# Performance work log

Hardware: AMD Instinct MI355X
Metric: run time of the kernel (lower is better)

The kernel has to match this reference:

```python
import jax, jax.numpy as jnp
import numpy as np

B, S, IN, H, D, STATE, PRED = 256, 512, 32, 256, 32, 4, 96


def setup_inputs() -> dict:
    key = jax.random.key(0)
    ks = jax.random.split(key, 16)
    sc = 1.0 / np.sqrt(H)

    def u(k, shape):
        return jax.random.uniform(k, shape, jnp.float32, -sc, sc)

    return {
        "x": jax.random.normal(ks[0], (B, S, IN), jnp.float32),
        # GRU layer 0
        "W_ih_l0": u(ks[1], (3 * H, IN)),
        "W_hh_l0": u(ks[2], (3 * H, H)),
        "b_ih_l0": u(ks[3], (3 * H,)),
        "b_hh_l0": u(ks[4], (3 * H,)),
        # GRU layer 1
        "W_ih_l1": u(ks[5], (3 * H, H)),
        "W_hh_l1": u(ks[6], (3 * H, H)),
        "b_ih_l1": u(ks[7], (3 * H,)),
        "b_hh_l1": u(ks[8], (3 * H,)),
        # state projection: hidden -> STATE*output_dim
        "W_proj": u(ks[9], (STATE * D, H)),
        "b_proj": u(ks[10], (STATE * D,)),
        # observation matrix, eye-initialized (output_dim, STATE)
        "C": jnp.eye(D, STATE, dtype=jnp.float32),
        "raw_level_decay": jnp.zeros((D,), jnp.float32),
        "raw_trend_decay": jnp.zeros((D,), jnp.float32),
        "raw_gamma": jnp.zeros((D,), jnp.float32),
        "omega": jnp.zeros((D,), jnp.float32),
    }


def _gru_layer(xs, W_ih, W_hh, b_ih, b_hh):
    # xs: (B, S, in_dim). Precompute input projections as one big GEMM.
    xp = jnp.einsum('bsi,gi->bsg', xs, W_ih) + b_ih  # (B, S, 3H)

    def step(h, xt):
        gh = h @ W_hh.T + b_hh  # (B, 3H)
        xr, xz, xn = jnp.split(xt, 3, axis=-1)
        hr, hz, hn = jnp.split(gh, 3, axis=-1)
        r = jax.nn.sigmoid(xr + hr)
        z = jax.nn.sigmoid(xz + hz)
        n = jnp.tanh(xn + r * hn)
        h_new = (1.0 - z) * n + z * h
        return h_new, h_new

    h0 = jnp.zeros((xs.shape[0], W_hh.shape[1]), xs.dtype)
    _, hs = jax.lax.scan(step, h0, jnp.swapaxes(xp, 0, 1))  # (S, B, H)
    return jnp.swapaxes(hs, 0, 1)  # (B, S, H)


def reference(x, W_ih_l0, W_hh_l0, b_ih_l0, b_hh_l0,
              W_ih_l1, W_hh_l1, b_ih_l1, b_hh_l1,
              W_proj, b_proj, C,
              raw_level_decay, raw_trend_decay, raw_gamma, omega):
    h1 = _gru_layer(x, W_ih_l0, W_hh_l0, b_ih_l0, b_hh_l0)
    h2 = _gru_layer(h1, W_ih_l1, W_hh_l1, b_ih_l1, b_hh_l1)
    final_h = h2[:, -1, :]  # (B, H)

    d_out = C.shape[0]
    s = (final_h @ W_proj.T + b_proj).reshape(x.shape[0], d_out, STATE)  # (B, D, 4)

    # time-invariant block-diagonal transition coefficients
    a_l = jax.nn.sigmoid(raw_level_decay) * 0.15 + 0.85
    a_t = jax.nn.sigmoid(raw_trend_decay) * 0.25 + 0.7
    g = jax.nn.sigmoid(raw_gamma) * 0.2 + 0.8
    c, sn = jnp.cos(omega), jnp.sin(omega)
    rot00, rot01 = g * c, -g * sn
    rot10, rot11 = g * sn, g * c

    def step(s, _):
        new_s = jnp.stack([
            s[..., 0] * a_l,
            s[..., 1] * a_t,
            s[..., 2] * rot00 + s[..., 3] * rot10,
            s[..., 2] * rot01 + s[..., 3] * rot11,
        ], axis=-1)
        y = jnp.einsum('ds,bds->bd', C, new_s)
        return new_s, y

    _, ys = jax.lax.scan(step, s, None, length=PRED)  # (PRED, B, D)
    return jnp.swapaxes(ys, 0, 1)  # (B, PRED, D)
```

## Files before the change

kernel.cpp:

```cpp
#include <hip/hip_runtime.h>
#include <cstdio>
#include <cstdint>

typedef _Float16 f16;
typedef f16 hf2   __attribute__((ext_vector_type(2)));
typedef f16 f16x8 __attribute__((ext_vector_type(8)));
typedef float f32x4 __attribute__((ext_vector_type(4)));
typedef unsigned int   u32;
typedef unsigned short u16;

#define B_    256
#define S_    512
#define IN_   32
#define H_    256
#define G3_   768
#define D_    32
#define PRED_ 96
#define TC_   32
#define KP_   72

#if __has_builtin(__builtin_amdgcn_fdot2)
__device__ __forceinline__ float fdot2(hf2 a, hf2 b, float c) {
  return __builtin_amdgcn_fdot2(a, b, c, false);
}
#else
__device__ __forceinline__ float fdot2(hf2 a, hf2 b, float c) {
  return c + (float)a[0] * (float)b[0] + (float)a[1] * (float)b[1];
}
#endif

__device__ __forceinline__ float sigm(float x) {
  return __builtin_amdgcn_rcpf(1.f + __expf(-x));
}
__device__ __forceinline__ float tanh_fast(float x) {
  return 1.f - 2.f * __builtin_amdgcn_rcpf(__expf(2.f * x) + 1.f);
}
__device__ __forceinline__ hf2 bc2(u32 v) { return __builtin_bit_cast(hf2, v); }

__global__ void f32_to_f16_k(const float* __restrict__ in, f16* __restrict__ out, int n) {
  int i = blockIdx.x * blockDim.x + threadIdx.x;
  if (i < n) out[i] = (f16)in[i];
}

__global__ void make_bias(const float* __restrict__ bih, const float* __restrict__ bhh,
                          float* __restrict__ out) {
  int i = blockIdx.x * blockDim.x + threadIdx.x;
  if (i < G3_) out[i] = bih[i] + (i < 512 ? bhh[i] : 0.f);
}

__device__ __forceinline__ f16x8 cvt8(const float* p) {
  float4 lo = ((const float4*)p)[0];
  float4 hi = ((const float4*)p)[1];
  f16x8 r;
  r[0] = (f16)lo.x; r[1] = (f16)lo.y; r[2] = (f16)lo.z; r[3] = (f16)lo.w;
  r[4] = (f16)hi.x; r[5] = (f16)hi.y; r[6] = (f16)hi.z; r[7] = (f16)hi.w;
  return r;
}

template <int KK>
__global__ __launch_bounds__(256) void gemm_xp(
    const void* __restrict__ Asrc, size_t aBlk, int tl_rows,
    const f16* __restrict__ Wih,
    const float* __restrict__ biasc,
    u16* __restrict__ xp) {
  const int tid = threadIdx.x;
  const int wv = tid >> 6, lane = tid & 63, lm = lane & 15, q = lane >> 4;
  const int tiles_pb = tl_rows >> 6;
  const int b = blockIdx.x / tiles_pb, hf = blockIdx.x % tiles_pb;
  const size_t arow0 = (size_t)b * aBlk + (size_t)(hf * 64) * KK;
  const size_t orow0 = (size_t)b * tl_rows + hf * 64;

#pragma unroll 1
  for (int nt = 0; nt < 12; ++nt) {
    const int n0 = wv * 192 + nt * 16;
    const f16* Bp = Wih + (size_t)(n0 + lm) * KK + q * 8;
    f32x4 acc[4];
#pragma unroll
    for (int j = 0; j < 4; ++j) acc[j] = f32x4{0.f, 0.f, 0.f, 0.f};
#pragma unroll
    for (int k0 = 0; k0 < KK; k0 += 32) {
      f16x8 bv = *(const f16x8*)(Bp + k0);
#pragma unroll
      for (int j = 0; j < 4; ++j) {
        f16x8 av;
        if constexpr (KK == 32) {
          av = cvt8((const float*)Asrc + arow0 + (size_t)(j * 16 + lm) * KK + k0 + q * 8);
        } else {
          av = *(const f16x8*)((const f16*)Asrc + arow0 + (size_t)(j * 16 + lm) * KK + k0 + q * 8);
        }
        acc[j] = __builtin_amdgcn_mfma_f32_16x16x32_f16(av, bv, acc[j], 0, 0, 0);
      }
    }
    const float bb = biasc[n0 + lm];
#pragma unroll
    for (int j = 0; j < 4; ++j)
#pragma unroll
      for (int r = 0; r < 4; ++r)
        xp[(orow0 + j * 16 + q * 4 + r) * G3_ + n0 + lm] =
            __builtin_bit_cast(u16, (f16)(acc[j][r] + bb));
  }
}

template <int LAYER>
__global__ __launch_bounds__(512, 2) void gru_rec(
    const u16* __restrict__ xp,
    const f16* __restrict__ Whh16,
    const float* __restrict__ bhh,
    float* __restrict__ hstate,
    f16* __restrict__ h1c,
    int tl_rows, int first) {
  const int b   = blockIdx.x;
  const int tid = threadIdx.x;
  const int p2 = tid >> 2, kh = tid & 3;
  const int u0 = p2 * 2;

  uint4 w0[3][8], w1[3][8];
#pragma unroll
  for (int g = 0; g < 3; ++g)
#pragma unroll
    for (int t = 0; t < 8; ++t) {
      w0[g][t] = ((const uint4*)Whh16)[(size_t)(g * 256 + u0) * 32 + kh * 8 + t];
      w1[g][t] = ((const uint4*)Whh16)[(size_t)(g * 256 + u0 + 1) * 32 + kh * 8 + t];
    }
  const int myu = u0 + kh;
  const float bhn = (kh < 2) ? bhh[512 + myu] : 0.f;

  __shared__ u16 xbuf[2][TC_ * G3_];
  __shared__ __align__(16) u16 hbuf[2][4 * KP_];
  __shared__ u16 hhist[TC_ * H_];

  float h = 0.f;
  if (kh < 2) {
    h = first ? 0.f : hstate[b * H_ + myu];
    hbuf[0][(myu >> 6) * KP_ + (myu & 63)] = __builtin_bit_cast(u16, (f16)h);
  }
  int cur = 0;
  const uint4* xsrc = (const uint4*)xp + (size_t)b * tl_rows * 96;
  const int nsub = tl_rows >> 5;

#pragma unroll 1
  for (int c2 = 0; c2 < nsub; ++c2) {
    {
      const uint4* src = xsrc + (size_t)c2 * 3072;
      uint4* dst = (uint4*)xbuf[c2 & 1];
#pragma unroll
      for (int pass = 0; pass < 2; ++pass) {
        uint4 v0 = src[(pass * 3 + 0) * 512 + tid];
        uint4 v1 = src[(pass * 3 + 1) * 512 + tid];
        uint4 v2 = src[(pass * 3 + 2) * 512 + tid];
        dst[(pass * 3 + 0) * 512 + tid] = v0;
        dst[(pass * 3 + 1) * 512 + tid] = v1;
        dst[(pass * 3 + 2) * 512 + tid] = v2;
      }
    }
    __syncthreads();
    const u16* xrow0 = xbuf[c2 & 1];

#pragma unroll 1
    for (int tl = 0; tl < TC_; ++tl) {
      const uint4* hb = (const uint4*)(hbuf[cur] + kh * KP_);
      float a0r = 0.f, a0z = 0.f, a0n = 0.f, a1r = 0.f, a1z = 0.f, a1n = 0.f;
#pragma unroll
      for (int cc = 0; cc < 8; ++cc) {
        uint4 hv = hb[cc];
        uint4 wa = w0[0][cc], wb = w0[1][cc], wc = w0[2][cc];
        uint4 wd = w1[0][cc], we = w1[1][cc], wf = w1[2][cc];
        a0r = fdot2(bc2(wa.x), bc2(hv.x), a0r);
        a0z = fdot2(bc2(wb.x), bc2(hv.x), a0z);
        a0n = fdot2(bc2(wc.x), bc2(hv.x), a0n);
        a1r = fdot2(bc2(wd.x), bc2(hv.x), a1r);
        a1z = fdot2(bc2(we.x), bc2(hv.x), a1z);
        a1n = fdot2(bc2(wf.x), bc2(hv.x), a1n);
        a0r = fdot2(bc2(wa.y), bc2(hv.y), a0r);
        a0z = fdot2(bc2(wb.y), bc2(hv.y), a0z);
        a0n = fdot2(bc2(wc.y), bc2(hv.y), a0n);
        a1r = fdot2(bc2(wd.y), bc2(hv.y), a1r);
        a1z = fdot2(bc2(we.y), bc2(hv.y), a1z);
        a1n = fdot2(bc2(wf.y), bc2(hv.y), a1n);
        a0r = fdot2(bc2(wa.z), bc2(hv.z), a0r);
        a0z = fdot2(bc2(wb.z), bc2(hv.z), a0z);
        a0n = fdot2(bc2(wc.z), bc2(hv.z), a0n);
        a1r = fdot2(bc2(wd.z), bc2(hv.z), a1r);
        a1z = fdot2(bc2(we.z), bc2(hv.z), a1z);
        a1n = fdot2(bc2(wf.z), bc2(hv.z), a1n);
        a0r = fdot2(bc2(wa.w), bc2(hv.w), a0r);
        a0z = fdot2(bc2(wb.w), bc2(hv.w), a0z);
        a0n = fdot2(bc2(wc.w), bc2(hv.w), a0n);
        a1r = fdot2(bc2(wd.w), bc2(hv.w), a1r);
        a1z = fdot2(bc2(we.w), bc2(hv.w), a1z);
        a1n = fdot2(bc2(wf.w), bc2(hv.w), a1n);
      }
      a0r += __shfl_xor(a0r, 1); a0r += __shfl_xor(a0r, 2);
      a0z += __shfl_xor(a0z, 1); a0z += __shfl_xor(a0z, 2);
      a0n += __shfl_xor(a0n, 1); a0n += __shfl_xor(a0n, 2);
      a1r += __shfl_xor(a1r, 1); a1r += __shfl_xor(a1r, 2);
      a1z += __shfl_xor(a1z, 1); a1z += __shfl_xor(a1z, 2);
      a1n += __shfl_xor(a1n, 1); a1n += __shfl_xor(a1n, 2);

      if (kh < 2) {
        const float ar = (kh == 0) ? a0r : a1r;
        const float az = (kh == 0) ? a0z : a1z;
        const float an = (kh == 0) ? a0n : a1n;
        const u16* xrow = xrow0 + tl * G3_;
        float xr = (float)__builtin_bit_cast(f16, xrow[myu]);
        float xz = (float)__builtin_bit_cast(f16, xrow[256 + myu]);
        float xn = (float)__builtin_bit_cast(f16, xrow[512 + myu]);
        float r = sigm(xr + ar);
        float z = sigm(xz + az);
        float n = tanh_fast(xn + r * (an + bhn));
        h = n + z * (h - n);
        const u16 h16v = __builtin_bit_cast(u16, (f16)h);
        hbuf[cur ^ 1][(myu >> 6) * KP_ + (myu & 63)] = h16v;
        if constexpr (LAYER == 0) hhist[tl * H_ + myu] = h16v;
      }
      __syncthreads();
      cur ^= 1;
    }

    if constexpr (LAYER == 0) {
      uint4 hv0 = ((const uint4*)hhist)[tid];
      uint4 hv1 = ((const uint4*)hhist)[512 + tid];
      uint4* dst = (uint4*)(h1c + ((size_t)b * tl_rows + c2 * TC_) * H_);
      dst[tid] = hv0;
      dst[512 + tid] = hv1;
    }
  }
  if (kh < 2) hstate[b * H_ + myu] = h;
}

__global__ __launch_bounds__(128) void proj_rollout(
    const float* __restrict__ hfinal, const float* __restrict__ Wp,
    const float* __restrict__ bp, const float* __restrict__ Cm,
    const float* __restrict__ rld, const float* __restrict__ rtd,
    const float* __restrict__ rg, const float* __restrict__ om,
    float* __restrict__ out) {
  const int b = blockIdx.x, tid = threadIdx.x;
  __shared__ float fh[256];
  __shared__ float sb[128];
  ((float2*)fh)[tid] = ((const float2*)(hfinal + b * 256))[tid];
  __syncthreads();
  const float4* wrow = (const float4*)(Wp + tid * 256);
  float acc = 0.f;
#pragma unroll 16
  for (int k4 = 0; k4 < 64; k4++) {
    float4 wv = wrow[k4];
    acc += wv.x * fh[4 * k4] + wv.y * fh[4 * k4 + 1] + wv.z * fh[4 * k4 + 2] +
           wv.w * fh[4 * k4 + 3];
  }
  sb[tid] = acc + bp[tid];
  __syncthreads();
  if (tid < 32) {
    const int dd = tid;
    float s0 = sb[dd * 4], s1 = sb[dd * 4 + 1], s2 = sb[dd * 4 + 2], s3 = sb[dd * 4 + 3];
    float al = sigm(rld[dd]) * 0.15f + 0.85f;
    float at = sigm(rtd[dd]) * 0.25f + 0.70f;
    float g  = sigm(rg[dd]) * 0.20f + 0.80f;
    float cw = cosf(om[dd]), sw = sinf(om[dd]);
    float r00 = g * cw, r01 = -g * sw, r10 = g * sw, r11 = g * cw;
    float c0 = Cm[dd * 4], c1 = Cm[dd * 4 + 1], c2 = Cm[dd * 4 + 2], c3 = Cm[dd * 4 + 3];
    float* op = out + (size_t)b * PRED_ * D_ + dd;
    for (int t = 0; t < PRED_; t++) {
      float n0 = s0 * al, n1 = s1 * at;
      float n2 = s2 * r00 + s3 * r10;
      float n3 = s2 * r01 + s3 * r11;
      op[(size_t)t * D_] = c0 * n0 + c1 * n1 + c2 * n2 + c3 * n3;
      s0 = n0; s1 = n1; s2 = n2; s3 = n3;
    }
  }
}

extern "C" void kernel_launch(void* const* d_in, const int* in_sizes, int n_in,
                              void* d_out, int out_size, void* d_ws,
                              size_t ws_size, hipStream_t stream) {
  (void)in_sizes; (void)n_in; (void)out_size;
  const float* x     = (const float*)d_in[0];
  const float* Wih0  = (const float*)d_in[1];
  const float* Whh0  = (const float*)d_in[2];
  const float* bih0  = (const float*)d_in[3];
  const float* bhh0  = (const float*)d_in[4];
  const float* Wih1  = (const float*)d_in[5];
  const float* Whh1  = (const float*)d_in[6];
  const float* bih1  = (const float*)d_in[7];
  const float* bhh1  = (const float*)d_in[8];
  const float* Wproj = (const float*)d_in[9];
  const float* bproj = (const float*)d_in[10];
  const float* Cm    = (const float*)d_in[11];
  const float* rld   = (const float*)d_in[12];
  const float* rtd   = (const float*)d_in[13];
  const float* rg    = (const float*)d_in[14];
  const float* om    = (const float*)d_in[15];
  float* out = (float*)d_out;

  char* ws = (char*)d_ws;
  const size_t wi0_off  = 0;
  const size_t wi1_off  = 49152;
  const size_t whh0_off = 442368;
  const size_t whh1_off = 835584;
  const size_t b0_off   = 1228800;
  const size_t b1_off   = 1231872;
  const size_t hs0_off  = 1234944;
  const size_t hs1_off  = 1497088;
  const size_t h1c_off  = 1759232;
  const size_t need64  = h1c_off + (size_t)B_ * 64 * H_ * 2  + (size_t)B_ * 64 * G3_ * 2;
  const size_t need128 = h1c_off + (size_t)B_ * 128 * H_ * 2 + (size_t)B_ * 128 * G3_ * 2;

  if (ws_size < need64) {
    fprintf(stderr, "kernel_launch: ws too small: have %zu need %zu — skipping\n",
            ws_size, need64);
    return;
  }
  const int TL = (ws_size >= need128) ? 128 : 64;
  const size_t xpc_off = h1c_off + (size_t)B_ * TL * H_ * 2;

  f16* wi016   = (f16*)(ws + wi0_off);
  f16* wi116   = (f16*)(ws + wi1_off);
  f16* whh016  = (f16*)(ws + whh0_off);
  f16* whh116  = (f16*)(ws + whh1_off);
  float* bias0 = (float*)(ws + b0_off);
  float* bias1 = (float*)(ws + b1_off);
  float* hst0  = (float*)(ws + hs0_off);
  float* hst1  = (float*)(ws + hs1_off);
  f16* h1c     = (f16*)(ws + h1c_off);
  u16* xpc     = (u16*)(ws + xpc_off);

  f32_to_f16_k<<<96, 256, 0, stream>>>(Wih0, wi016, G3_ * IN_);
  f32_to_f16_k<<<768, 256, 0, stream>>>(Wih1, wi116, G3_ * H_);
  f32_to_f16_k<<<768, 256, 0, stream>>>(Whh0, whh016, G3_ * H_);
  f32_to_f16_k<<<768, 256, 0, stream>>>(Whh1, whh116, G3_ * H_);
  make_bias<<<3, 256, 0, stream>>>(bih0, bhh0, bias0);
  make_bias<<<3, 256, 0, stream>>>(bih1, bhh1, bias1);

  const int nchunks = S_ / TL;
  const int gblocks = B_ * (TL / 64);
  for (int c = 0; c < nchunks; ++c) {
    gemm_xp<IN_><<<gblocks, 256, 0, stream>>>(
        (const void*)(x + (size_t)c * TL * IN_), (size_t)S_ * IN_, TL, wi016, bias0, xpc);
    gru_rec<0><<<B_, 512, 0, stream>>>(xpc, whh016, bhh0, hst0, h1c, TL, c == 0);
    gemm_xp<H_><<<gblocks, 256, 0, stream>>>(
        (const void*)h1c, (size_t)TL * H_, TL, wi116, bias1, xpc);
    gru_rec<1><<<B_, 512, 0, stream>>>(xpc, whh116, bhh1, hst1, nullptr, TL, c == 0);
  }
  proj_rollout<<<B_, 128, 0, stream>>>(hst1, Wproj, bproj, Cm, rld, rtd, rg, om, out);
}
```

Measured before the change: 1.640 ms.

## Pipeline GRU layers so layer 0 and layer 1 chunks run in one launch

Merges the two recurrent kernels into one role-dispatched kernel. It launches 2*B blocks, so layer 0 on chunk c runs at the same time as layer 1 on chunk c-1, with separate xp buffers for each layer. This is meant to cut the serial recurrence path roughly in half by filling idle CUs with the second layer's work. To keep two blocks resident per CU, the LDS sub-chunk is halved and its double buffer is dropped, and the chunk length is fixed at 64. The cost is more per-sub-chunk syncs, a larger fixed workspace requirement, and more kernel launches.

```diff
diff --git a/kernel.cpp b/kernel.cpp
--- a/kernel.cpp
+++ b/kernel.cpp
@@ -16,7 +16,7 @@
 #define G3_   768
 #define D_    32
 #define PRED_ 96
-#define TC_   32
+#define TC_   16
 #define KP_   72
 
 #if __has_builtin(__builtin_amdgcn_fdot2)
@@ -101,15 +101,25 @@
   }
 }
 
-template <int LAYER>
-__global__ __launch_bounds__(512, 2) void gru_rec(
-    const u16* __restrict__ xp,
-    const f16* __restrict__ Whh16,
-    const float* __restrict__ bhh,
-    float* __restrict__ hstate,
+__global__ __launch_bounds__(512, 2) void gru_rec2(
+    const u16* __restrict__ xp0,
+    const u16* __restrict__ xp1,
+    const f16* __restrict__ W0,
+    const f16* __restrict__ W1,
+    const float* __restrict__ bhh0,
+    const float* __restrict__ bhh1,
+    float* __restrict__ hst0,
+    float* __restrict__ hst1,
     f16* __restrict__ h1c,
-    int tl_rows, int first) {
-  const int b   = blockIdx.x;
+    int tl, int first0, int first1, int nwg0) {
+  const int role = (int)(blockIdx.x >= (unsigned)nwg0);
+  const int b = blockIdx.x - (role ? nwg0 : 0);
+  const u16* xp = role ? xp1 : xp0;
+  const f16* Whh16 = role ? W1 : W0;
+  const float* bhh = role ? bhh1 : bhh0;
+  float* hstate = role ? hst1 : hst0;
+  const int first = role ? first1 : first0;
+
   const int tid = threadIdx.x;
   const int p2 = tid >> 2, kh = tid & 3;
   const int u0 = p2 * 2;
@@ -125,7 +135,7 @@
   const int myu = u0 + kh;
   const float bhn = (kh < 2) ? bhh[512 + myu] : 0.f;
 
-  __shared__ u16 xbuf[2][TC_ * G3_];
+  __shared__ u16 xbuf[TC_ * G3_];
   __shared__ __align__(16) u16 hbuf[2][4 * KP_];
   __shared__ u16 hhist[TC_ * H_];
 
@@ -135,29 +145,21 @@
     hbuf[0][(myu >> 6) * KP_ + (myu & 63)] = __builtin_bit_cast(u16, (f16)h);
   }
   int cur = 0;
-  const uint4* xsrc = (const uint4*)xp + (size_t)b * tl_rows * 96;
-  const int nsub = tl_rows >> 5;
+  const uint4* xsrc = (const uint4*)xp + (size_t)b * tl * 96;
+  const int nsub = tl / TC_;
 
 #pragma unroll 1
   for (int c2 = 0; c2 < nsub; ++c2) {
     {
-      const uint4* src = xsrc + (size_t)c2 * 3072;
-      uint4* dst = (uint4*)xbuf[c2 & 1];
-#pragma unroll
-      for (int pass = 0; pass < 2; ++pass) {
-        uint4 v0 = src[(pass * 3 + 0) * 512 + tid];
-        uint4 v1 = src[(pass * 3 + 1) * 512 + tid];
-        uint4 v2 = src[(pass * 3 + 2) * 512 + tid];
-        dst[(pass * 3 + 0) * 512 + tid] = v0;
-        dst[(pass * 3 + 1) * 512 + tid] = v1;
-        dst[(pass * 3 + 2) * 512 + tid] = v2;
-      }
+      const uint4* src = xsrc + (size_t)c2 * 1536;
+      uint4* dst = (uint4*)xbuf;
+      uint4 v0 = src[tid], v1 = src[512 + tid], v2 = src[1024 + tid];
+      dst[tid] = v0; dst[512 + tid] = v1; dst[1024 + tid] = v2;
     }
     __syncthreads();
-    const u16* xrow0 = xbuf[c2 & 1];
 
 #pragma unroll 1
-    for (int tl = 0; tl < TC_; ++tl) {
+    for (int tl_i = 0; tl_i < TC_; ++tl_i) {
       const uint4* hb = (const uint4*)(hbuf[cur] + kh * KP_);
       float a0r = 0.f, a0z = 0.f, a0n = 0.f, a1r = 0.f, a1z = 0.f, a1n = 0.f;
 #pragma unroll
@@ -201,7 +203,7 @@
         const float ar = (kh == 0) ? a0r : a1r;
         const float az = (kh == 0) ? a0z : a1z;
         const float an = (kh == 0) ? a0n : a1n;
-        const u16* xrow = xrow0 + tl * G3_;
+        const u16* xrow = xbuf + tl_i * G3_;
         float xr = (float)__builtin_bit_cast(f16, xrow[myu]);
         float xz = (float)__builtin_bit_cast(f16, xrow[256 + myu]);
         float xn = (float)__builtin_bit_cast(f16, xrow[512 + myu]);
@@ -211,18 +213,15 @@
         h = n + z * (h - n);
         const u16 h16v = __builtin_bit_cast(u16, (f16)h);
         hbuf[cur ^ 1][(myu >> 6) * KP_ + (myu & 63)] = h16v;
-        if constexpr (LAYER == 0) hhist[tl * H_ + myu] = h16v;
+        if (!role) hhist[tl_i * H_ + myu] = h16v;
       }
       __syncthreads();
       cur ^= 1;
     }
 
-    if constexpr (LAYER == 0) {
+    if (!role) {
       uint4 hv0 = ((const uint4*)hhist)[tid];
-      uint4 hv1 = ((const uint4*)hhist)[512 + tid];
-      uint4* dst = (uint4*)(h1c + ((size_t)b * tl_rows + c2 * TC_) * H_);
-      dst[tid] = hv0;
-      dst[512 + tid] = hv1;
+      ((uint4*)(h1c + ((size_t)b * tl + c2 * TC_) * H_))[tid] = hv0;
     }
   }
   if (kh < 2) hstate[b * H_ + myu] = h;
@@ -292,6 +291,7 @@
   float* out = (float*)d_out;
 
   char* ws = (char*)d_ws;
+  const int TL = 64;
   const size_t wi0_off  = 0;
   const size_t wi1_off  = 49152;
   const size_t whh0_off = 442368;
@@ -301,16 +301,15 @@
   const size_t hs0_off  = 1234944;
   const size_t hs1_off  = 1497088;
   const size_t h1c_off  = 1759232;
-  const size_t need64  = h1c_off + (size_t)B_ * 64 * H_ * 2  + (size_t)B_ * 64 * G3_ * 2;
-  const size_t need128 = h1c_off + (size_t)B_ * 128 * H_ * 2 + (size_t)B_ * 128 * G3_ * 2;
-
-  if (ws_size < need64) {
+  const size_t xp0_off  = 10147840;
+  const size_t xp1_off  = 35313664;
+  const size_t need     = 60479488;
+
+  if (ws_size < need) {
     fprintf(stderr, "kernel_launch: ws too small: have %zu need %zu — skipping\n",
-            ws_size, need64);
+            ws_size, need);
     return;
   }
-  const int TL = (ws_size >= need128) ? 128 : 64;
-  const size_t xpc_off = h1c_off + (size_t)B_ * TL * H_ * 2;
 
   f16* wi016   = (f16*)(ws + wi0_off);
   f16* wi116   = (f16*)(ws + wi1_off);
@@ -321,7 +320,8 @@
   float* hst0  = (float*)(ws + hs0_off);
   float* hst1  = (float*)(ws + hs1_off);
   f16* h1c     = (f16*)(ws + h1c_off);
-  u16* xpc     = (u16*)(ws + xpc_off);
+  u16* xp0     = (u16*)(ws + xp0_off);
+  u16* xp1     = (u16*)(ws + xp1_off);
 
   f32_to_f16_k<<<96, 256, 0, stream>>>(Wih0, wi016, G3_ * IN_);
   f32_to_f16_k<<<768, 256, 0, stream>>>(Wih1, wi116, G3_ * H_);
@@ -331,14 +331,21 @@
   make_bias<<<3, 256, 0, stream>>>(bih1, bhh1, bias1);
 
   const int nchunks = S_ / TL;
-  const int gblocks = B_ * (TL / 64);
-  for (int c = 0; c < nchunks; ++c) {
-    gemm_xp<IN_><<<gblocks, 256, 0, stream>>>(
-        (const void*)(x + (size_t)c * TL * IN_), (size_t)S_ * IN_, TL, wi016, bias0, xpc);
-    gru_rec<0><<<B_, 512, 0, stream>>>(xpc, whh016, bhh0, hst0, h1c, TL, c == 0);
-    gemm_xp<H_><<<gblocks, 256, 0, stream>>>(
-        (const void*)h1c, (size_t)TL * H_, TL, wi116, bias1, xpc);
-    gru_rec<1><<<B_, 512, 0, stream>>>(xpc, whh116, bhh1, hst1, nullptr, TL, c == 0);
-  }
+  gemm_xp<IN_><<<B_, 256, 0, stream>>>(
+      (const void*)x, (size_t)S_ * IN_, TL, wi016, bias0, xp0);
+  gru_rec2<<<B_, 512, 0, stream>>>(xp0, xp1, whh016, whh116, bhh0, bhh1,
+                                   hst0, hst1, h1c, TL, 1, 0, B_);
+  for (int c = 1; c < nchunks; ++c) {
+    gemm_xp<H_><<<B_, 256, 0, stream>>>(
+        (const void*)h1c, (size_t)TL * H_, TL, wi116, bias1, xp1);
+    gemm_xp<IN_><<<B_, 256, 0, stream>>>(
+        (const void*)(x + (size_t)c * TL * IN_), (size_t)S_ * IN_, TL, wi016, bias0, xp0);
+    gru_rec2<<<2 * B_, 512, 0, stream>>>(xp0, xp1, whh016, whh116, bhh0, bhh1,
+                                         hst0, hst1, h1c, TL, 0, (c == 1) ? 1 : 0, B_);
+  }
+  gemm_xp<H_><<<B_, 256, 0, stream>>>(
+      (const void*)h1c, (size_t)TL * H_, TL, wi116, bias1, xp1);
+  gru_rec2<<<B_, 512, 0, stream>>>(xp0, xp1, whh016, whh116, bhh0, bhh1,
+                                   hst0, hst1, h1c, TL, 0, 0, 0);
   proj_rollout<<<B_, 128, 0, stream>>>(hst1, Wproj, bproj, Cm, rld, rtd, rg, om, out);
 }
```

New measurement: 1.802 ms. +9.9%, slower.
